# Optimization experiments

Hardware: AMD Instinct MI355X
Metric: run time of the kernel (lower is better)

The kernel has to match this reference:

```python
import jax, jax.numpy as jnp
import numpy as np

B, T, F_IN = 32, 2000, 1024
GROUPS, NUM_VARS, VQ_DIM = 2, 320, 256
VAR_DIM = VQ_DIM // GROUPS  # 128
TAU = 2.0  # curr_temp = max_temp at step 0
EPS = 1e-7


def setup_inputs() -> dict:
    key = jax.random.key(0)
    k1, k2, k3, k4 = jax.random.split(key, 4)
    x = jax.random.normal(k1, (B, T, F_IN), jnp.float32)
    # nn.Linear: weight ~ N(0,1) per module init, bias zeros
    proj_w = jax.random.normal(k2, (GROUPS * NUM_VARS, F_IN), jnp.float32)
    proj_b = jnp.zeros((GROUPS * NUM_VARS,), jnp.float32)
    # nn.init.uniform_ on vars (leading singleton dim dropped)
    codebook = jax.random.uniform(k3, (GROUPS * NUM_VARS, VAR_DIM), jnp.float32)
    # pre-sampled standard Gumbel noise (training-path gumbel_softmax)
    u = jax.random.uniform(k4, (B * T, GROUPS * NUM_VARS), jnp.float32, 1e-6, 1.0 - 1e-6)
    gumbel = -jnp.log(-jnp.log(u))
    return {"x": x, "proj_w": proj_w, "proj_b": proj_b, "codebook": codebook, "gumbel": gumbel}


def reference(x, proj_w, proj_b, codebook, gumbel):
    bsz, tsz, fsz = x.shape
    bt = bsz * tsz
    logits = x.reshape(bt, fsz) @ proj_w.T + proj_b                 # [BT, G*V]
    lg = logits.reshape(bt, GROUPS, NUM_VARS)                       # [BT, G, V]

    # hard codes (argmax of raw logits) -> code perplexity
    k = jnp.argmax(lg, axis=-1)                                     # [BT, G]
    hard_x = jax.nn.one_hot(k, NUM_VARS, dtype=lg.dtype)            # [BT, G, V]
    hard_probs = hard_x.mean(axis=0)                                # [G, V]
    code_perplexity = jnp.exp(-jnp.sum(hard_probs * jnp.log(hard_probs + EPS), -1)).sum()

    avg_probs = jax.nn.softmax(lg, axis=-1).mean(axis=0)            # [G, V]
    prob_perplex = jnp.exp(-jnp.sum(avg_probs * jnp.log(avg_probs + EPS), -1)).sum()

    # training path: gumbel_softmax(tau, hard=True) with straight-through
    g = gumbel.reshape(bt, GROUPS, NUM_VARS)
    y_soft = jax.nn.softmax((lg + g) / TAU, axis=-1)                # [BT, G, V]
    y_hard = jax.nn.one_hot(jnp.argmax(y_soft, -1), NUM_VARS, dtype=y_soft.dtype)
    y = y_hard + y_soft - jax.lax.stop_gradient(y_soft)             # straight-through

    # codebook weighted sum; original does (one_hot[...,None] * vars).sum over V
    cb = codebook.reshape(GROUPS, NUM_VARS, VAR_DIM)
    q = jnp.einsum("tgv,gvd->tgd", y, cb)                           # [BT, G, var_dim]
    q = q.reshape(bsz, tsz, VQ_DIM)
    return q, code_perplexity, prob_perplex
```

## Files before the change

kernel.cpp:

```cpp
#include <hip/hip_runtime.h>
#include <cstdint>
#include <cstddef>

#define BT_TOT 64000
#define FIN    1024
#define GV     640
#define NV     320
#define VD     128
#define INV_BT (1.0f/64000.0f)

#define WTILE_B 40960
#define BUF_B 49152

typedef __attribute__((ext_vector_type(8))) __bf16 bf16x8;
typedef __attribute__((ext_vector_type(16))) float f32x16;

typedef __attribute__((address_space(1))) void gvoid_t;
typedef __attribute__((address_space(3))) void lvoid_t;

__device__ inline short f2bf(float x) {
    unsigned int u = __float_as_uint(x);
    unsigned int r = (u + 0x7fffu + ((u >> 16) & 1u)) >> 16;
    return (short)r;
}
__device__ inline float bf2f(short h) {
    return __uint_as_float(((unsigned int)(unsigned short)h) << 16);
}
__device__ inline bf16x8 ld_frag(const short* p) {
    union { uint4 u; bf16x8 v; } t;
    t.u = *(const uint4*)p;
    return t.v;
}
__device__ __forceinline__ void glds16(const void* g, void* l) {
    __builtin_amdgcn_global_load_lds((gvoid_t*)g, (lvoid_t*)l, 16, 0, 0);
}

__global__ __launch_bounds__(256) void prep(
    const float* __restrict__ W, char* __restrict__ Wpk,
    float* __restrict__ psum_g, int* __restrict__ cnt_g)
{
    const int t = blockIdx.x * 256 + threadIdx.x;
    if (t < GV) { psum_g[t] = 0.f; cnt_g[t] = 0; }
    const int r   = t >> 7;
    const int ck8 = t & 127;
    const int kt  = ck8 >> 1;
    const int ch  = ck8 & 1;
    const float* src = W + (size_t)r * FIN + (size_t)ck8 * 8;
    const float4 a = ((const float4*)src)[0];
    const float4 b = ((const float4*)src)[1];
    float xs[8] = {a.x, a.y, a.z, a.w, b.x, b.y, b.z, b.w};
    short hi[8], lo[8];
#pragma unroll
    for (int e = 0; e < 8; ++e) {
        hi[e] = f2bf(xs[e]);
        lo[e] = f2bf(xs[e] - bf2f(hi[e]));
    }
    char* dst = Wpk + (size_t)kt * WTILE_B + (size_t)r * 32 + ch * 16;
    *(uint4*)dst             = *(uint4*)hi;
    *(uint4*)(dst + 20480)   = *(uint4*)lo;
}

__global__ __launch_bounds__(512, 2) void fused(
    const float* __restrict__ X, const char* __restrict__ Wpk,
    const float* __restrict__ bias, const float* __restrict__ gumbel,
    const float* __restrict__ codebook, float* __restrict__ q,
    float* __restrict__ psum_g, int* __restrict__ cnt_g)
{
    __shared__ __align__(16) char smem[2 * BUF_B];

    const int tid  = threadIdx.x;
    const int lane = tid & 63, wave = tid >> 6;
    const int mw = wave & 3, nw = wave >> 2;
    const int cl = lane & 31, h = lane >> 5;
    const int row0 = blockIdx.x * 128;

    const int ar  = tid >> 2;
    const int akq = (tid & 3) * 4;

    f32x16 acc[10];
#pragma unroll
    for (int nt = 0; nt < 10; ++nt) acc[nt] = (f32x16)0.0f;

    {
#pragma unroll
        for (int i = 0; i < 5; ++i) {
            const int task = tid + 512 * i;
            glds16(Wpk + (size_t)task * 16, smem + 8192 + task * 16);
        }
        const float4 xa = *(const float4*)(X + (size_t)(row0 + ar) * FIN + akq);
        float xs[4] = {xa.x, xa.y, xa.z, xa.w};
        short hi4[4], lo4[4];
#pragma unroll
        for (int e = 0; e < 4; ++e) {
            hi4[e] = f2bf(xs[e]);
            lo4[e] = f2bf(xs[e] - bf2f(hi4[e]));
        }
        *(short4*)(smem + ar * 32 + akq * 2)        = make_short4(hi4[0], hi4[1], hi4[2], hi4[3]);
        *(short4*)(smem + 4096 + ar * 32 + akq * 2) = make_short4(lo4[0], lo4[1], lo4[2], lo4[3]);
    }
    __syncthreads();

    for (int t = 0; t < 64; ++t) {
        const int c = t & 1;
        char* bufc = smem + c * BUF_B;
        char* bufn = smem + (c ^ 1) * BUF_B;
        const bool more = (t < 63);
        float4 xa;
        if (more) {
            const char* wt = Wpk + (size_t)(t + 1) * WTILE_B;
#pragma unroll
            for (int i = 0; i < 5; ++i) {
                const int task = tid + 512 * i;
                glds16(wt + (size_t)task * 16, bufn + 8192 + task * 16);
            }
            xa = *(const float4*)(X + (size_t)(row0 + ar) * FIN + (t + 1) * 16 + akq);
        }

        __builtin_amdgcn_s_setprio(1);
        const int arow = mw * 32 + cl;
        const bf16x8 a_h = ld_frag((const short*)(bufc + arow * 32 + h * 16));
        const bf16x8 a_l = ld_frag((const short*)(bufc + 4096 + arow * 32 + h * 16));
#pragma unroll
        for (int nt = 0; nt < 10; ++nt) {
            const int bcol = nw * 320 + nt * 32 + cl;
            const bf16x8 b_h = ld_frag((const short*)(bufc + 8192 + bcol * 32 + h * 16));
            const bf16x8 b_l = ld_frag((const short*)(bufc + 8192 + 20480 + bcol * 32 + h * 16));
            acc[nt] = __builtin_amdgcn_mfma_f32_32x32x16_bf16(a_h, b_h, acc[nt], 0, 0, 0);
            acc[nt] = __builtin_amdgcn_mfma_f32_32x32x16_bf16(a_l, b_h, acc[nt], 0, 0, 0);
            acc[nt] = __builtin_amdgcn_mfma_f32_32x32x16_bf16(a_h, b_l, acc[nt], 0, 0, 0);
        }
        __builtin_amdgcn_s_setprio(0);

        if (more) {
            float xs[4] = {xa.x, xa.y, xa.z, xa.w};
            short hi4[4], lo4[4];
#pragma unroll
            for (int e = 0; e < 4; ++e) {
                hi4[e] = f2bf(xs[e]);
                lo4[e] = f2bf(xs[e] - bf2f(hi4[e]));
            }
            *(short4*)(bufn + ar * 32 + akq * 2)        = make_short4(hi4[0], hi4[1], hi4[2], hi4[3]);
            *(short4*)(bufn + 4096 + ar * 32 + akq * 2) = make_short4(lo4[0], lo4[1], lo4[2], lo4[3]);
        }
        __syncthreads();
    }

    float* psum_l = (float*)(smem);
    int*   cnt_l  = (int*)(smem + 2560);
    int*   gidx   = (int*)(smem + 5120);

    for (int i = tid; i < GV; i += 512) { psum_l[i] = 0.f; cnt_l[i] = 0; }
    __syncthreads();

#pragma unroll
    for (int nt = 0; nt < 10; ++nt) {
        const float bv = bias[nw * 320 + nt * 32 + cl];
#pragma unroll
        for (int r = 0; r < 16; ++r) acc[nt][r] += bv;
    }

    float pcol[10];
#pragma unroll
    for (int nt = 0; nt < 10; ++nt) pcol[nt] = 0.f;

#pragma unroll
    for (int reg = 0; reg < 16; ++reg) {
        const int rloc = mw * 32 + (reg & 3) + 8 * (reg >> 2) + 4 * h;
        const float* gp = gumbel + (size_t)(row0 + rloc) * GV + nw * 320;
        float bestv = -3.4e38f, gbv = -3.4e38f;
        int bestc = 0, gbc = 0;
#pragma unroll
        for (int nt = 0; nt < 10; ++nt) {
            const float v = acc[nt][reg];
            const int cc = nt * 32 + cl;
            const float tv = v + gp[cc];
            if (v > bestv) { bestv = v; bestc = cc; }
            if (tv > gbv)  { gbv = tv;  gbc = cc; }
        }
#pragma unroll
        for (int off = 1; off < 32; off <<= 1) {
            const float v2 = __shfl_xor(bestv, off); const int c2 = __shfl_xor(bestc, off);
            if (v2 > bestv || (v2 == bestv && c2 < bestc)) { bestv = v2; bestc = c2; }
            const float g2 = __shfl_xor(gbv, off); const int gc2 = __shfl_xor(gbc, off);
            if (g2 > gbv || (g2 == gbv && gc2 < gbc)) { gbv = g2; gbc = gc2; }
        }
        float e[10], s = 0.f;
#pragma unroll
        for (int nt = 0; nt < 10; ++nt) { e[nt] = __expf(acc[nt][reg] - bestv); s += e[nt]; }
#pragma unroll
        for (int off = 1; off < 32; off <<= 1) s += __shfl_xor(s, off);
        const float inv_s = 1.0f / s;
#pragma unroll
        for (int nt = 0; nt < 10; ++nt) pcol[nt] += e[nt] * inv_s;
        if (cl == 0) {
            atomicAdd(&cnt_l[nw * 320 + bestc], 1);
            gidx[rloc * 2 + nw] = nw * 320 + gbc;
        }
    }
#pragma unroll
    for (int nt = 0; nt < 10; ++nt) {
        const float v = pcol[nt] + __shfl_xor(pcol[nt], 32);
        if (h == 0) atomicAdd(&psum_l[nw * 320 + nt * 32 + cl], v);
    }
    __syncthreads();

    {
        const int unit = tid >> 1, half = tid & 1;
        const int row = unit >> 1, gq = unit & 1;
        const int idx = gidx[row * 2 + gq];
        const float4* srcp = (const float4*)(codebook + (size_t)idx * VD + half * 64);
        float4* dstp = (float4*)(q + (size_t)(row0 + row) * 256 + gq * VD + half * 64);
#pragma unroll
        for (int i = 0; i < 16; ++i) dstp[i] = srcp[i];
    }
    for (int i = tid; i < GV; i += 512) {
        atomicAdd(&psum_g[i], psum_l[i]);
        atomicAdd(&cnt_g[i], cnt_l[i]);
    }
}

__global__ void finalize(const int* __restrict__ cnt_g, const float* __restrict__ psum_g,
                         float* __restrict__ out_scalars)
{
    const int lane = threadIdx.x;
    float hsum[2] = {0.f, 0.f}, p[2] = {0.f, 0.f};
    for (int i = lane; i < GV; i += 64) {
        const int g = i / NV;
        const float hp = (float)cnt_g[i] * INV_BT;
        const float ap = psum_g[i] * INV_BT;
        hsum[g] -= hp * logf(hp + 1e-7f);
        p[g]    -= ap * logf(ap + 1e-7f);
    }
#pragma unroll
    for (int off = 32; off > 0; off >>= 1) {
        hsum[0] += __shfl_xor(hsum[0], off); hsum[1] += __shfl_xor(hsum[1], off);
        p[0] += __shfl_xor(p[0], off);       p[1] += __shfl_xor(p[1], off);
    }
    if (lane == 0) {
        out_scalars[0] = expf(hsum[0]) + expf(hsum[1]);
        out_scalars[1] = expf(p[0]) + expf(p[1]);
    }
}

extern "C" void kernel_launch(void* const* d_in, const int* in_sizes, int n_in,
                              void* d_out, int out_size, void* d_ws, size_t ws_size,
                              hipStream_t stream)
{
    const float* X  = (const float*)d_in[0];
    const float* W  = (const float*)d_in[1];
    const float* Bv = (const float*)d_in[2];
    const float* CB = (const float*)d_in[3];
    const float* GU = (const float*)d_in[4];

    float* q = (float*)d_out;
    float* out_scalars = (float*)d_out + (size_t)BT_TOT * 256;

    char* ws = (char*)d_ws;
    float* psum_g = (float*)ws;
    int*   cnt_g  = (int*)(ws + 4096);
    char*  Wpk    = ws + 8192;

    prep<<<320, 256, 0, stream>>>(W, Wpk, psum_g, cnt_g);
    fused<<<500, 512, 0, stream>>>(X, Wpk, Bv, GU, CB, q, psum_g, cnt_g);
    finalize<<<1, 64, 0, stream>>>(cnt_g, psum_g, out_scalars);
}
```

Before: 719.2 us.

## Load X fragments directly into registers and drop LDS staging for A operand

```diff
diff --git a/kernel.cpp b/kernel.cpp
--- a/kernel.cpp
+++ b/kernel.cpp
@@ -10,7 +10,6 @@
 #define INV_BT (1.0f/64000.0f)
 
 #define WTILE_B 40960
-#define BUF_B 49152
 
 typedef __attribute__((ext_vector_type(8))) __bf16 bf16x8;
 typedef __attribute__((ext_vector_type(16))) float f32x16;
@@ -66,83 +65,78 @@
     const float* __restrict__ codebook, float* __restrict__ q,
     float* __restrict__ psum_g, int* __restrict__ cnt_g)
 {
-    __shared__ __align__(16) char smem[2 * BUF_B];
+    __shared__ __align__(16) char smem[2 * WTILE_B];
 
     const int tid  = threadIdx.x;
     const int lane = tid & 63, wave = tid >> 6;
     const int mw = wave & 3, nw = wave >> 2;
     const int cl = lane & 31, h = lane >> 5;
     const int row0 = blockIdx.x * 128;
-
-    const int ar  = tid >> 2;
-    const int akq = (tid & 3) * 4;
+    const int arow = mw * 32 + cl;
 
     f32x16 acc[10];
 #pragma unroll
     for (int nt = 0; nt < 10; ++nt) acc[nt] = (f32x16)0.0f;
 
+    const float* aptr = X + (size_t)(row0 + arow) * FIN + h * 8;
+
+    float4 xa0, xa1;
     {
 #pragma unroll
         for (int i = 0; i < 5; ++i) {
             const int task = tid + 512 * i;
-            glds16(Wpk + (size_t)task * 16, smem + 8192 + task * 16);
-        }
-        const float4 xa = *(const float4*)(X + (size_t)(row0 + ar) * FIN + akq);
-        float xs[4] = {xa.x, xa.y, xa.z, xa.w};
-        short hi4[4], lo4[4];
-#pragma unroll
-        for (int e = 0; e < 4; ++e) {
-            hi4[e] = f2bf(xs[e]);
-            lo4[e] = f2bf(xs[e] - bf2f(hi4[e]));
-        }
-        *(short4*)(smem + ar * 32 + akq * 2)        = make_short4(hi4[0], hi4[1], hi4[2], hi4[3]);
-        *(short4*)(smem + 4096 + ar * 32 + akq * 2) = make_short4(lo4[0], lo4[1], lo4[2], lo4[3]);
-    }
-    __syncthreads();
+            glds16(Wpk + (size_t)task * 16, smem + task * 16);
+        }
+        __builtin_amdgcn_sched_barrier(0);
+        xa0 = *(const float4*)(aptr);
+        xa1 = *(const float4*)(aptr + 4);
+    }
 
     for (int t = 0; t < 64; ++t) {
-        const int c = t & 1;
-        char* bufc = smem + c * BUF_B;
-        char* bufn = smem + (c ^ 1) * BUF_B;
-        const bool more = (t < 63);
-        float4 xa;
-        if (more) {
+        asm volatile("s_waitcnt vmcnt(2)" ::: "memory");
+        __builtin_amdgcn_s_barrier();
+
+        const char* bufc = smem + (t & 1) * WTILE_B;
+        float4 na0, na1;
+        if (t < 63) {
+            char* bufn = smem + ((t + 1) & 1) * WTILE_B;
             const char* wt = Wpk + (size_t)(t + 1) * WTILE_B;
 #pragma unroll
             for (int i = 0; i < 5; ++i) {
                 const int task = tid + 512 * i;
-                glds16(wt + (size_t)task * 16, bufn + 8192 + task * 16);
+                glds16(wt + (size_t)task * 16, bufn + task * 16);
             }
-            xa = *(const float4*)(X + (size_t)(row0 + ar) * FIN + (t + 1) * 16 + akq);
-        }
+            __builtin_amdgcn_sched_barrier(0);
+            const float* ap = aptr + (t + 1) * 16;
+            na0 = *(const float4*)(ap);
+            na1 = *(const float4*)(ap + 4);
+        }
+        __builtin_amdgcn_sched_barrier(0);
+
+        union { float4 f[2]; float s[8]; } ua;
+        ua.f[0] = xa0; ua.f[1] = xa1;
+        union { short s[8]; bf16x8 v; } uh, ul;
+#pragma unroll
+        for (int e = 0; e < 8; ++e) {
+            const short hb = f2bf(ua.s[e]);
+            uh.s[e] = hb;
+            ul.s[e] = f2bf(ua.s[e] - bf2f(hb));
+        }
+        const bf16x8 a_h = uh.v, a_l = ul.v;
 
         __builtin_amdgcn_s_setprio(1);
-        const int arow = mw * 32 + cl;
-        const bf16x8 a_h = ld_frag((const short*)(bufc + arow * 32 + h * 16));
-        const bf16x8 a_l = ld_frag((const short*)(bufc + 4096 + arow * 32 + h * 16));
 #pragma unroll
         for (int nt = 0; nt < 10; ++nt) {
             const int bcol = nw * 320 + nt * 32 + cl;
-            const bf16x8 b_h = ld_frag((const short*)(bufc + 8192 + bcol * 32 + h * 16));
-            const bf16x8 b_l = ld_frag((const short*)(bufc + 8192 + 20480 + bcol * 32 + h * 16));
+            const bf16x8 b_h = ld_frag((const short*)(bufc + bcol * 32 + h * 16));
+            const bf16x8 b_l = ld_frag((const short*)(bufc + 20480 + bcol * 32 + h * 16));
             acc[nt] = __builtin_amdgcn_mfma_f32_32x32x16_bf16(a_h, b_h, acc[nt], 0, 0, 0);
             acc[nt] = __builtin_amdgcn_mfma_f32_32x32x16_bf16(a_l, b_h, acc[nt], 0, 0, 0);
             acc[nt] = __builtin_amdgcn_mfma_f32_32x32x16_bf16(a_h, b_l, acc[nt], 0, 0, 0);
         }
         __builtin_amdgcn_s_setprio(0);
 
-        if (more) {
-            float xs[4] = {xa.x, xa.y, xa.z, xa.w};
-            short hi4[4], lo4[4];
-#pragma unroll
-            for (int e = 0; e < 4; ++e) {
-                hi4[e] = f2bf(xs[e]);
-                lo4[e] = f2bf(xs[e] - bf2f(hi4[e]));
-            }
-            *(short4*)(bufn + ar * 32 + akq * 2)        = make_short4(hi4[0], hi4[1], hi4[2], hi4[3]);
-            *(short4*)(bufn + 4096 + ar * 32 + akq * 2) = make_short4(lo4[0], lo4[1], lo4[2], lo4[3]);
-        }
-        __syncthreads();
+        xa0 = na0; xa1 = na1;
     }
 
     float* psum_l = (float*)(smem);
```

New measurement: 719.4 us. Within noise of the previous version (+0.0%).
